# Kernel tuning notes

Measured on AMD Instinct MI355X. Metric: run time of the kernel, lower is better.

The kernel has to match this reference:

```python
import jax, jax.numpy as jnp
import numpy as np

N, E = 50000, 800000
IN_DIM, HID, HEADS, NUM_CLASSES, NUM_GRAPHS, NUM_LAYERS = 64, 64, 4, 10000, 256, 3
OUT_W = HID * HEADS  # 256


def _gat_layer(x, src, dst, W, a_src, a_dst, b, n_nodes):
    # x: [N, in], W: [heads*out, in], a_src/a_dst: [heads, out], b: [heads*out]
    h = (x @ W.T).reshape(n_nodes, HEADS, HID)            # [N, H, D]
    s_src = jnp.einsum('nhd,hd->nh', h, a_src)            # [N, H]
    s_dst = jnp.einsum('nhd,hd->nh', h, a_dst)
    alpha = jax.nn.leaky_relu(s_src[src] + s_dst[dst], 0.2)  # [E, H]
    m = jax.ops.segment_max(alpha, dst, num_segments=n_nodes)
    m = jnp.where(jnp.isfinite(m), m, 0.0)                # isolated-node safety
    ex = jnp.exp(alpha - m[dst])
    denom = jax.ops.segment_sum(ex, dst, num_segments=n_nodes)
    w = ex / (denom[dst] + 1e-16)                         # PyG softmax epsilon
    out = jax.ops.segment_sum(h[src] * w[:, :, None], dst, num_segments=n_nodes)
    return out.reshape(n_nodes, HEADS * HID) + b


def setup_inputs() -> dict:
    key = jax.random.key(0)
    ks = jax.random.split(key, 20)
    inp = {
        'x': jax.random.normal(ks[0], (N, IN_DIM), jnp.float32),
        'edge_index': jax.random.randint(ks[1], (2, E), 0, N, jnp.int32),
        'batch': jnp.sort(jax.random.randint(ks[2], (N,), 0, NUM_GRAPHS, jnp.int32)),
        'class_label': jax.random.randint(ks[3], (NUM_GRAPHS,), 0, NUM_CLASSES, jnp.int32),
        'emb': jax.random.normal(ks[4], (NUM_CLASSES, HID), jnp.float32),
    }
    in_dims = [IN_DIM + HID, OUT_W, OUT_W]
    for l in range(NUM_LAYERS):
        kw = jax.random.split(ks[5 + l], 4)
        d_in = in_dims[l]
        sc = 1.0 / np.sqrt(d_in)
        inp[f'W{l}'] = jax.random.uniform(kw[0], (OUT_W, d_in), jnp.float32, -sc, sc)
        inp[f'asrc{l}'] = jax.random.uniform(kw[1], (HEADS, HID), jnp.float32, -sc, sc)
        inp[f'adst{l}'] = jax.random.uniform(kw[2], (HEADS, HID), jnp.float32, -sc, sc)
        inp[f'b{l}'] = jnp.zeros((OUT_W,), jnp.float32)
    sc = 1.0 / np.sqrt(OUT_W)
    inp['cls_W'] = jax.random.uniform(ks[10], (1, OUT_W), jnp.float32, -sc, sc)
    inp['cls_b'] = jnp.zeros((1,), jnp.float32)
    return inp


def reference(x, edge_index, batch, class_label, emb,
              W0, asrc0, adst0, b0,
              W1, asrc1, adst1, b1,
              W2, asrc2, adst2, b2,
              cls_W, cls_b):
    n = x.shape[0]
    # template embedding aligned per node
    t = emb[class_label][batch]                          # [N, HID]
    h = jnp.concatenate([x, t], axis=-1)                 # [N, IN+HID]
    # PyG GATConv adds self-loops by default
    loop = jnp.arange(n, dtype=edge_index.dtype)
    src = jnp.concatenate([edge_index[0], loop])
    dst = jnp.concatenate([edge_index[1], loop])
    params = [(W0, asrc0, adst0, b0), (W1, asrc1, adst1, b1), (W2, asrc2, adst2, b2)]
    for (W, a_s, a_d, b) in params:
        h = _gat_layer(h, src, dst, W, a_s, a_d, b, n)
        h = jax.nn.leaky_relu(h, 0.01)                   # F.leaky_relu default slope
    return h @ cls_W.T + cls_b                           # [N, 1]
```

## Files before the change

kernel.cpp:

```cpp
#include <hip/hip_runtime.h>
#include <hip/hip_fp16.h>
#include <math.h>

#define NNODES 50000
#define NEDGES 800000
#define NT_TILES (((NNODES + 127) / 128) * 2)
#define NGROUPS ((NNODES + 3) / 4)
#define NH0 (NNODES * 128)
#define NH04 (NH0 / 4)
#define NW4 (163840 / 4)
#define NDEG4 (NNODES / 4)
#define NPREP4 (NH04 + NW4 + NDEG4)

typedef __attribute__((ext_vector_type(8))) _Float16 f16x8;
typedef __attribute__((ext_vector_type(4))) _Float16 f16x4;
typedef __attribute__((ext_vector_type(4))) float f32x4;

static __device__ __forceinline__ void gl_lds16(const void* g, void* l) {
    __builtin_amdgcn_global_load_lds(
        (const __attribute__((address_space(1))) void*)g,
        (__attribute__((address_space(3))) void*)l, 16, 0, 0);
}

static __device__ __forceinline__ float sel4(float4 v, int head) {
    float r = v.x;
    r = (head == 1) ? v.y : r;
    r = (head == 2) ? v.z : r;
    r = (head == 3) ? v.w : r;
    return r;
}

__global__ void prep_kernel(const float* __restrict__ x,
                            const int* __restrict__ batch,
                            const int* __restrict__ class_label,
                            const float* __restrict__ emb,
                            const float* __restrict__ W0,
                            const float* __restrict__ W1,
                            const float* __restrict__ W2,
                            _Float16* __restrict__ h0,
                            _Float16* __restrict__ F0,
                            _Float16* __restrict__ F1,
                            _Float16* __restrict__ F2,
                            int* __restrict__ deg) {
    int i4 = blockIdx.x * blockDim.x + threadIdx.x;
    if (i4 < NH04) {
        int idx = i4 * 4;
        int n = idx >> 7, c = idx & 127;
        float4 v;
        if (c < 64) v = *(const float4*)&x[(n << 6) + c];
        else        v = *(const float4*)&emb[class_label[batch[n]] * 64 + (c - 64)];
        f16x4 h = {(_Float16)v.x, (_Float16)v.y, (_Float16)v.z, (_Float16)v.w};
        *(f16x4*)&h0[idx] = h;
    } else if (i4 < NH04 + NW4) {
        int i = (i4 - NH04) * 4;
        const float* src; _Float16* dst;
        if (i < 32768)       { src = W0 + i;           dst = F0 + i; }
        else if (i < 98304)  { src = W1 + (i - 32768); dst = F1 + (i - 32768); }
        else                 { src = W2 + (i - 98304); dst = F2 + (i - 98304); }
        float4 v = *(const float4*)src;
        f16x4 h = {(_Float16)v.x, (_Float16)v.y, (_Float16)v.z, (_Float16)v.w};
        *(f16x4*)dst = h;
    } else if (i4 < NPREP4) {
        int j = (i4 - NH04 - NW4) * 4;
        int4 z = {0, 0, 0, 0};
        *(int4*)&deg[j] = z;
    }
}

template <int K>
static __device__ void gemm_tile_dev(const _Float16* __restrict__ A,
                                     const _Float16* __restrict__ W,
                                     const float* __restrict__ a_src,
                                     const float* __restrict__ a_dst,
                                     _Float16* __restrict__ Cf,
                                     float* __restrict__ ssrc,
                                     float* __restrict__ sdst,
                                     char* smem, int bm, int bn) {
    const int M = NNODES;
    int tid = threadIdx.x;
    int lane = tid & 63, wave = tid >> 6;
    int wm = wave >> 1, wn = wave & 1;
    int l16 = lane & 15, quad = lane >> 4;
    int rsub = lane >> 3;
    int kcs = (lane & 7) ^ rsub;
    int sw = l16 & 7;

    f32x4 acc[4][4];
#pragma unroll
    for (int r = 0; r < 4; ++r)
#pragma unroll
        for (int c = 0; c < 4; ++c) acc[r][c] = (f32x4){0.f, 0.f, 0.f, 0.f};

    const int NST = K / 64;
    auto issue = [&](int buf, int s) {
        _Float16* dA = (_Float16*)(smem + buf * 32768);
        _Float16* dB = (_Float16*)(smem + buf * 32768 + 16384);
        int ks = s * 64;
#pragma unroll
        for (int j = 0; j < 4; ++j) {
            int seg = wave * 4 + j;
            int r = seg * 8 + rsub;
            int acol = ks + kcs * 8;
            int garow = bm + r; if (garow > M - 1) garow = M - 1;
            gl_lds16(A + (size_t)garow * K + acol, &dA[seg * 512]);
            gl_lds16(W + (size_t)(bn + r) * K + acol, &dB[seg * 512]);
        }
    };

    issue(0, 0);
    __syncthreads();
#pragma unroll
    for (int s = 0; s < NST; ++s) {
        if (s + 1 < NST) issue((s + 1) & 1, s + 1);
        const _Float16* sA = (const _Float16*)(smem + (s & 1) * 32768);
        const _Float16* sB = (const _Float16*)(smem + (s & 1) * 32768 + 16384);
#pragma unroll
        for (int ks32 = 0; ks32 < 2; ++ks32) {
            f16x8 af[4], bf[4];
#pragma unroll
            for (int r = 0; r < 4; ++r) {
                int row = wm * 64 + r * 16 + l16;
                af[r] = *(const f16x8*)&sA[row * 64 + ((ks32 * 4 + quad) ^ sw) * 8];
            }
#pragma unroll
            for (int c = 0; c < 4; ++c) {
                int row = wn * 64 + c * 16 + l16;
                bf[c] = *(const f16x8*)&sB[row * 64 + ((ks32 * 4 + quad) ^ sw) * 8];
            }
#pragma unroll
            for (int r = 0; r < 4; ++r)
#pragma unroll
                for (int c = 0; c < 4; ++c)
                    acc[r][c] = __builtin_amdgcn_mfma_f32_16x16x32_f16(
                        bf[c], af[r], acc[r][c], 0, 0, 0);
        }
        __syncthreads();
    }

    int headblk = (bn + wn * 64) >> 6;
    f32x4 av[4], dv[4];
#pragma unroll
    for (int c = 0; c < 4; ++c) {
        av[c] = *(const f32x4*)&a_src[headblk * 64 + c * 16 + quad * 4];
        dv[c] = *(const f32x4*)&a_dst[headblk * 64 + c * 16 + quad * 4];
    }
#pragma unroll
    for (int r = 0; r < 4; ++r) {
        int grow = bm + wm * 64 + r * 16 + l16;
        bool ok = grow < M;
        float ps = 0.f, pd = 0.f;
#pragma unroll
        for (int c = 0; c < 4; ++c) {
            f32x4 a = acc[r][c];
            ps += a[0] * av[c][0] + a[1] * av[c][1]
                + a[2] * av[c][2] + a[3] * av[c][3];
            pd += a[0] * dv[c][0] + a[1] * dv[c][1]
                + a[2] * dv[c][2] + a[3] * dv[c][3];
            if (ok) {
                f16x4 hv = {(_Float16)a[0], (_Float16)a[1],
                            (_Float16)a[2], (_Float16)a[3]};
                *(f16x4*)&Cf[(size_t)grow * 256 + bn + wn * 64 + c * 16 + quad * 4] = hv;
            }
        }
        ps += __shfl_xor(ps, 16, 64);
        ps += __shfl_xor(ps, 32, 64);
        pd += __shfl_xor(pd, 16, 64);
        pd += __shfl_xor(pd, 32, 64);
        if (quad == 0 && ok) {
            ssrc[grow * 4 + headblk] = ps;
            sdst[grow * 4 + headblk] = pd;
        }
    }
}

template <int K>
__global__ __launch_bounds__(256) void gemm_mfma_kernel(
        const _Float16* __restrict__ A, const _Float16* __restrict__ W,
        const float* __restrict__ a_src, const float* __restrict__ a_dst,
        _Float16* __restrict__ Cf,
        float* __restrict__ ssrc, float* __restrict__ sdst) {
    __shared__ __align__(16) char smem[65536];
    gemm_tile_dev<K>(A, W, a_src, a_dst, Cf, ssrc, sdst, smem,
                     blockIdx.x * 128, blockIdx.y * 128);
}

__global__ __launch_bounds__(256) void gemm0_bucket_kernel(
        const _Float16* __restrict__ A, const _Float16* __restrict__ W,
        const float* __restrict__ a_src, const float* __restrict__ a_dst,
        _Float16* __restrict__ Cf,
        float* __restrict__ ssrc, float* __restrict__ sdst,
        const int* __restrict__ ei,
        int* __restrict__ deg, int* __restrict__ slots) {
    __shared__ __align__(16) char smem[65536];
    int b = blockIdx.x;
    if ((b & 1) == 0) {
        int tile = b >> 1;
        if (tile < NT_TILES)
            gemm_tile_dev<128>(A, W, a_src, a_dst, Cf, ssrc, sdst, smem,
                               (tile >> 1) * 128, (tile & 1) * 128);
    } else {
        int rel = b >> 1;
        int stride = NT_TILES * 256;
        for (int e = rel * 256 + (int)threadIdx.x; e < NEDGES; e += stride) {
            int d = ei[NEDGES + e];
            int pos = atomicAdd(&deg[d], 1);
            if (pos < 64) slots[(size_t)d * 64 + pos] = ei[e];
        }
    }
}

template <bool LAST>
__global__ __launch_bounds__(256) void aggregate_kernel(
        const _Float16* __restrict__ hpf,
        const float* __restrict__ ssrc,
        const float* __restrict__ sdst,
        const int* __restrict__ deg,
        const int* __restrict__ slots,
        const float* __restrict__ bias,
        _Float16* __restrict__ out_h,
        const float* __restrict__ cls_W,
        const float* __restrict__ cls_b,
        float* __restrict__ out) {
    __shared__ __align__(16) float s_w[4][64][4];
    __shared__ int s_idx[4][64];
    int lane = threadIdx.x & 63;
    int slot = threadIdx.x >> 6;
    int n = blockIdx.x * 4 + slot;
    if (n >= NNODES) return;
    int head = lane >> 4;
    int dn = deg[n]; if (dn > 64) dn = 64;
    float4 sd = ((const float4*)sdst)[n];
    const f16x4* hp4 = (const f16x4*)hpf;

    float4 ssl = ((const float4*)ssrc)[n];
    float ax = ssl.x + sd.x, ay = ssl.y + sd.y;
    float az = ssl.z + sd.z, aw = ssl.w + sd.w;
    ax = ax > 0.f ? ax : 0.2f * ax;
    ay = ay > 0.f ? ay : 0.2f * ay;
    az = az > 0.f ? az : 0.2f * az;
    aw = aw > 0.f ? aw : 0.2f * aw;
    float4 exs = {__expf(ax), __expf(ay), __expf(az), __expf(aw)};
    float wself = sel4(exs, head);
    f16x4 vs = hp4[(size_t)n * 64 + lane];
    float dsum = wself;
    float4 acc = {wself * (float)vs.x, wself * (float)vs.y,
                  wself * (float)vs.z, wself * (float)vs.w};

    float4 ex = {0.f, 0.f, 0.f, 0.f};
    int s = 0;
    if (lane < dn) {
        s = slots[(size_t)n * 64 + lane];
        float4 ss = ((const float4*)ssrc)[s];
        float bx = ss.x + sd.x, by = ss.y + sd.y;
        float bz = ss.z + sd.z, bw = ss.w + sd.w;
        bx = bx > 0.f ? bx : 0.2f * bx;
        by = by > 0.f ? by : 0.2f * by;
        bz = bz > 0.f ? bz : 0.2f * bz;
        bw = bw > 0.f ? bw : 0.2f * bw;
        ex.x = __expf(bx); ex.y = __expf(by);
        ex.z = __expf(bz); ex.w = __expf(bw);
    }
    *(float4*)&s_w[slot][lane][0] = ex;
    s_idx[slot][lane] = s;

    int e = 0;
    for (; e + 8 <= dn; e += 8) {
        int si[8]; float w[8]; f16x4 v[8];
#pragma unroll
        for (int t = 0; t < 8; ++t) {
            si[t] = s_idx[slot][e + t];
            w[t] = s_w[slot][e + t][head];
        }
#pragma unroll
        for (int t = 0; t < 8; ++t) v[t] = hp4[(size_t)si[t] * 64 + lane];
#pragma unroll
        for (int t = 0; t < 8; ++t) {
            dsum += w[t];
            acc.x += w[t] * (float)v[t].x;
            acc.y += w[t] * (float)v[t].y;
            acc.z += w[t] * (float)v[t].z;
            acc.w += w[t] * (float)v[t].w;
        }
    }
    for (; e < dn; ++e) {
        int si = s_idx[slot][e];
        float w = s_w[slot][e][head];
        f16x4 v = hp4[(size_t)si * 64 + lane];
        dsum += w;
        acc.x += w * (float)v.x; acc.y += w * (float)v.y;
        acc.z += w * (float)v.z; acc.w += w * (float)v.w;
    }

    float inv = 1.f / (dsum + 1e-16f);
    float4 bv = ((const float4*)bias)[lane];
    float4 o;
    o.x = acc.x * inv + bv.x;
    o.y = acc.y * inv + bv.y;
    o.z = acc.z * inv + bv.z;
    o.w = acc.w * inv + bv.w;
    o.x = o.x > 0.f ? o.x : 0.01f * o.x;
    o.y = o.y > 0.f ? o.y : 0.01f * o.y;
    o.z = o.z > 0.f ? o.z : 0.01f * o.z;
    o.w = o.w > 0.f ? o.w : 0.01f * o.w;

    if (!LAST) {
        f16x4 ov = {(_Float16)o.x, (_Float16)o.y, (_Float16)o.z, (_Float16)o.w};
        ((f16x4*)out_h)[(size_t)n * 64 + lane] = ov;
    } else {
        float4 wv = ((const float4*)cls_W)[lane];
        float sdot = o.x * wv.x + o.y * wv.y + o.z * wv.z + o.w * wv.w;
#pragma unroll
        for (int off = 1; off < 64; off <<= 1)
            sdot += __shfl_xor(sdot, off, 64);
        if (lane == 0) out[n] = sdot + cls_b[0];
    }
}

extern "C" void kernel_launch(void* const* d_in, const int* in_sizes, int n_in,
                              void* d_out, int out_size, void* d_ws, size_t ws_size,
                              hipStream_t stream) {
    const float* x     = (const float*)d_in[0];
    const int*   ei    = (const int*)d_in[1];
    const int*   batch = (const int*)d_in[2];
    const int*   clab  = (const int*)d_in[3];
    const float* emb   = (const float*)d_in[4];
    const float* W[3]    = {(const float*)d_in[5], (const float*)d_in[9],  (const float*)d_in[13]};
    const float* asrc[3] = {(const float*)d_in[6], (const float*)d_in[10], (const float*)d_in[14]};
    const float* adst[3] = {(const float*)d_in[7], (const float*)d_in[11], (const float*)d_in[15]};
    const float* bias[3] = {(const float*)d_in[8], (const float*)d_in[12], (const float*)d_in[16]};
    const float* clsW = (const float*)d_in[17];
    const float* clsb = (const float*)d_in[18];
    float* out = (float*)d_out;

    char* ws = (char*)d_ws;
    size_t off = 0;
    auto alloc = [&](size_t bytes) {
        void* p = ws + off;
        off += (bytes + 255) & ~(size_t)255;
        return p;
    };
    _Float16* Cf   = (_Float16*)alloc((size_t)NNODES * 256 * 2);
    _Float16* hA   = (_Float16*)alloc((size_t)NNODES * 256 * 2);
    _Float16* h0f  = (_Float16*)alloc((size_t)NNODES * 128 * 2);
    _Float16* Wf[3];
    Wf[0] = (_Float16*)alloc((size_t)256 * 128 * 2);
    Wf[1] = (_Float16*)alloc((size_t)256 * 256 * 2);
    Wf[2] = (_Float16*)alloc((size_t)256 * 256 * 2);
    float* ssrc  = (float*)alloc((size_t)NNODES * 4 * 4);
    float* sdst  = (float*)alloc((size_t)NNODES * 4 * 4);
    int*   deg   = (int*)alloc((size_t)NNODES * 4);
    int*   slots = (int*)alloc((size_t)NNODES * 64 * 4);
    (void)ws_size; (void)in_sizes; (void)n_in; (void)out_size;

    prep_kernel<<<dim3((NPREP4 + 255) / 256), dim3(256), 0, stream>>>(
        x, batch, clab, emb, W[0], W[1], W[2], h0f, Wf[0], Wf[1], Wf[2], deg);

    dim3 gemm_grid((NNODES + 127) / 128, 2);
    dim3 node_grid(NGROUPS);

    gemm0_bucket_kernel<<<dim3(NT_TILES * 2), dim3(256), 0, stream>>>(
        h0f, Wf[0], asrc[0], adst[0], Cf, ssrc, sdst, ei, deg, slots);
    aggregate_kernel<false><<<node_grid, dim3(256), 0, stream>>>(
        Cf, ssrc, sdst, deg, slots, bias[0], hA, nullptr, nullptr, nullptr);

    gemm_mfma_kernel<256><<<gemm_grid, dim3(256), 0, stream>>>(
        hA, Wf[1], asrc[1], adst[1], Cf, ssrc, sdst);
    aggregate_kernel<false><<<node_grid, dim3(256), 0, stream>>>(
        Cf, ssrc, sdst, deg, slots, bias[1], hA, nullptr, nullptr, nullptr);

    gemm_mfma_kernel<256><<<gemm_grid, dim3(256), 0, stream>>>(
        hA, Wf[2], asrc[2], adst[2], Cf, ssrc, sdst);
    aggregate_kernel<true><<<node_grid, dim3(256), 0, stream>>>(
        Cf, ssrc, sdst, deg, slots, bias[2], nullptr, clsW, clsb, out);
}
```

Baseline: 373.3 us.

## Software-pipeline neighbor gathers, precompute byte offsets in slots, raise occupancy hint

```diff
diff --git a/kernel.cpp b/kernel.cpp
--- a/kernel.cpp
+++ b/kernel.cpp
@@ -1,6 +1,7 @@
 #include <hip/hip_runtime.h>
 #include <hip/hip_fp16.h>
 #include <math.h>
+#include <stdint.h>
 
 #define NNODES 50000
 #define NEDGES 800000
@@ -204,13 +205,13 @@
         for (int e = rel * 256 + (int)threadIdx.x; e < NEDGES; e += stride) {
             int d = ei[NEDGES + e];
             int pos = atomicAdd(&deg[d], 1);
-            if (pos < 64) slots[(size_t)d * 64 + pos] = ei[e];
+            if (pos < 64) slots[(size_t)d * 64 + pos] = ei[e] << 9;
         }
     }
 }
 
 template <bool LAST>
-__global__ __launch_bounds__(256) void aggregate_kernel(
+__global__ __launch_bounds__(256, 8) void aggregate_kernel(
         const _Float16* __restrict__ hpf,
         const float* __restrict__ ssrc,
         const float* __restrict__ sdst,
@@ -228,9 +229,10 @@
     int n = blockIdx.x * 4 + slot;
     if (n >= NNODES) return;
     int head = lane >> 4;
+    uint32_t lane8 = (uint32_t)lane * 8u;
+    const char* hbase = (const char*)hpf;
     int dn = deg[n]; if (dn > 64) dn = 64;
     float4 sd = ((const float4*)sdst)[n];
-    const f16x4* hp4 = (const f16x4*)hpf;
 
     float4 ssl = ((const float4*)ssrc)[n];
     float ax = ssl.x + sd.x, ay = ssl.y + sd.y;
@@ -241,16 +243,16 @@
     aw = aw > 0.f ? aw : 0.2f * aw;
     float4 exs = {__expf(ax), __expf(ay), __expf(az), __expf(aw)};
     float wself = sel4(exs, head);
-    f16x4 vs = hp4[(size_t)n * 64 + lane];
+    f16x4 vs = *(const f16x4*)(hbase + (((uint32_t)n << 9) + lane8));
     float dsum = wself;
     float4 acc = {wself * (float)vs.x, wself * (float)vs.y,
                   wself * (float)vs.z, wself * (float)vs.w};
 
     float4 ex = {0.f, 0.f, 0.f, 0.f};
-    int s = 0;
+    int soff = 0;
     if (lane < dn) {
-        s = slots[(size_t)n * 64 + lane];
-        float4 ss = ((const float4*)ssrc)[s];
+        soff = slots[(size_t)n * 64 + lane];
+        float4 ss = *(const float4*)((const char*)ssrc + ((uint32_t)soff >> 5));
         float bx = ss.x + sd.x, by = ss.y + sd.y;
         float bz = ss.z + sd.z, bw = ss.w + sd.w;
         bx = bx > 0.f ? bx : 0.2f * bx;
@@ -261,34 +263,47 @@
         ex.z = __expf(bz); ex.w = __expf(bw);
     }
     *(float4*)&s_w[slot][lane][0] = ex;
-    s_idx[slot][lane] = s;
-
-    int e = 0;
-    for (; e + 8 <= dn; e += 8) {
-        int si[8]; float w[8]; f16x4 v[8];
+    s_idx[slot][lane] = soff;
+
+    auto loadb = [&](int eb, f16x4* v, float* w) {
 #pragma unroll
         for (int t = 0; t < 8; ++t) {
-            si[t] = s_idx[slot][e + t];
-            w[t] = s_w[slot][e + t][head];
-        }
-#pragma unroll
-        for (int t = 0; t < 8; ++t) v[t] = hp4[(size_t)si[t] * 64 + lane];
+            uint32_t off = (uint32_t)s_idx[slot][eb + t] + lane8;
+            v[t] = *(const f16x4*)(hbase + off);
+            w[t] = s_w[slot][eb + t][head];
+        }
+    };
+    auto accum = [&](const f16x4* v, const float* w) {
 #pragma unroll
         for (int t = 0; t < 8; ++t) {
-            dsum += w[t];
-            acc.x += w[t] * (float)v[t].x;
-            acc.y += w[t] * (float)v[t].y;
-            acc.z += w[t] * (float)v[t].z;
-            acc.w += w[t] * (float)v[t].w;
-        }
-    }
-    for (; e < dn; ++e) {
-        int si = s_idx[slot][e];
-        float w = s_w[slot][e][head];
-        f16x4 v = hp4[(size_t)si * 64 + lane];
-        dsum += w;
-        acc.x += w * (float)v.x; acc.y += w * (float)v.y;
-        acc.z += w * (float)v.z; acc.w += w * (float)v.w;
+            float wt = w[t];
+            dsum += wt;
+            acc.x += wt * (float)v[t].x;
+            acc.y += wt * (float)v[t].y;
+            acc.z += wt * (float)v[t].z;
+            acc.w += wt * (float)v[t].w;
+        }
+    };
+
+    int B = (dn + 7) >> 3;
+    if (B) {
+        f16x4 va[8], vb[8];
+        float wa[8], wb[8];
+        loadb(0, va, wa);
+        int i = 1;
+        for (; i + 1 < B; i += 2) {
+            loadb(i * 8, vb, wb);
+            accum(va, wa);
+            loadb((i + 1) * 8, va, wa);
+            accum(vb, wb);
+        }
+        if (i < B) {
+            loadb(i * 8, vb, wb);
+            accum(va, wa);
+            accum(vb, wb);
+        } else {
+            accum(va, wa);
+        }
     }
 
     float inv = 1.f / (dsum + 1e-16f);
```

Measured after the change: 408.5 us. 9.4% more time.

## Split aggregation into weight-packing and column-sliced gather kernels with sliced layout

Applied to the files above, without the earlier changes.

```diff
diff --git a/kernel.cpp b/kernel.cpp
--- a/kernel.cpp
+++ b/kernel.cpp
@@ -1,6 +1,7 @@
 #include <hip/hip_runtime.h>
 #include <hip/hip_fp16.h>
 #include <math.h>
+#include <stdint.h>
 
 #define NNODES 50000
 #define NEDGES 800000
@@ -10,7 +11,8 @@
 #define NH04 (NH0 / 4)
 #define NW4 (163840 / 4)
 #define NDEG4 (NNODES / 4)
-#define NPREP4 (NH04 + NW4 + NDEG4)
+#define NSELF4 (NNODES / 4)
+#define NPREP4 (NH04 + NW4 + NDEG4 + NSELF4)
 
 typedef __attribute__((ext_vector_type(8))) _Float16 f16x8;
 typedef __attribute__((ext_vector_type(4))) _Float16 f16x4;
@@ -20,14 +22,6 @@
     __builtin_amdgcn_global_load_lds(
         (const __attribute__((address_space(1))) void*)g,
         (__attribute__((address_space(3))) void*)l, 16, 0, 0);
-}
-
-static __device__ __forceinline__ float sel4(float4 v, int head) {
-    float r = v.x;
-    r = (head == 1) ? v.y : r;
-    r = (head == 2) ? v.z : r;
-    r = (head == 3) ? v.w : r;
-    return r;
 }
 
 __global__ void prep_kernel(const float* __restrict__ x,
@@ -41,7 +35,8 @@
                             _Float16* __restrict__ F0,
                             _Float16* __restrict__ F1,
                             _Float16* __restrict__ F2,
-                            int* __restrict__ deg) {
+                            int* __restrict__ deg,
+                            int* __restrict__ slots) {
     int i4 = blockIdx.x * blockDim.x + threadIdx.x;
     if (i4 < NH04) {
         int idx = i4 * 4;
@@ -60,10 +55,16 @@
         float4 v = *(const float4*)src;
         f16x4 h = {(_Float16)v.x, (_Float16)v.y, (_Float16)v.z, (_Float16)v.w};
         *(f16x4*)dst = h;
+    } else if (i4 < NH04 + NW4 + NDEG4) {
+        int j = (i4 - NH04 - NW4) * 4;
+        int4 o = {1, 1, 1, 1};
+        *(int4*)&deg[j] = o;
     } else if (i4 < NPREP4) {
-        int j = (i4 - NH04 - NW4) * 4;
-        int4 z = {0, 0, 0, 0};
-        *(int4*)&deg[j] = z;
+        int j = (i4 - NH04 - NW4 - NDEG4) * 4;
+        slots[(size_t)(j + 0) * 64] = j + 0;
+        slots[(size_t)(j + 1) * 64] = j + 1;
+        slots[(size_t)(j + 2) * 64] = j + 2;
+        slots[(size_t)(j + 3) * 64] = j + 3;
     }
 }
 
@@ -157,9 +158,10 @@
             pd += a[0] * dv[c][0] + a[1] * dv[c][1]
                 + a[2] * dv[c][2] + a[3] * dv[c][3];
             if (ok) {
+                int col = bn + wn * 64 + c * 16 + quad * 4;
                 f16x4 hv = {(_Float16)a[0], (_Float16)a[1],
                             (_Float16)a[2], (_Float16)a[3]};
-                *(f16x4*)&Cf[(size_t)grow * 256 + bn + wn * 64 + c * 16 + quad * 4] = hv;
+                *(f16x4*)&Cf[((size_t)(col >> 5) * NNODES + grow) * 32 + (col & 31)] = hv;
             }
         }
         ps += __shfl_xor(ps, 16, 64);
@@ -209,48 +211,26 @@
     }
 }
 
-template <bool LAST>
-__global__ __launch_bounds__(256) void aggregate_kernel(
-        const _Float16* __restrict__ hpf,
+__global__ __launch_bounds__(256) void weights_kernel(
         const float* __restrict__ ssrc,
         const float* __restrict__ sdst,
         const int* __restrict__ deg,
         const int* __restrict__ slots,
-        const float* __restrict__ bias,
-        _Float16* __restrict__ out_h,
-        const float* __restrict__ cls_W,
-        const float* __restrict__ cls_b,
-        float* __restrict__ out) {
-    __shared__ __align__(16) float s_w[4][64][4];
-    __shared__ int s_idx[4][64];
+        unsigned* __restrict__ pk,
+        float* __restrict__ out,
+        const float* __restrict__ cls_b) {
     int lane = threadIdx.x & 63;
-    int slot = threadIdx.x >> 6;
-    int n = blockIdx.x * 4 + slot;
-    if (n >= NNODES) return;
-    int head = lane >> 4;
+    int wv = threadIdx.x >> 6;
+    int n = blockIdx.x * 4 + wv;
     int dn = deg[n]; if (dn > 64) dn = 64;
+    int dnp = (dn + 7) & ~7;
     float4 sd = ((const float4*)sdst)[n];
-    const f16x4* hp4 = (const f16x4*)hpf;
-
-    float4 ssl = ((const float4*)ssrc)[n];
-    float ax = ssl.x + sd.x, ay = ssl.y + sd.y;
-    float az = ssl.z + sd.z, aw = ssl.w + sd.w;
-    ax = ax > 0.f ? ax : 0.2f * ax;
-    ay = ay > 0.f ? ay : 0.2f * ay;
-    az = az > 0.f ? az : 0.2f * az;
-    aw = aw > 0.f ? aw : 0.2f * aw;
-    float4 exs = {__expf(ax), __expf(ay), __expf(az), __expf(aw)};
-    float wself = sel4(exs, head);
-    f16x4 vs = hp4[(size_t)n * 64 + lane];
-    float dsum = wself;
-    float4 acc = {wself * (float)vs.x, wself * (float)vs.y,
-                  wself * (float)vs.z, wself * (float)vs.w};
 
     float4 ex = {0.f, 0.f, 0.f, 0.f};
-    int s = 0;
+    int id = 0;
     if (lane < dn) {
-        s = slots[(size_t)n * 64 + lane];
-        float4 ss = ((const float4*)ssrc)[s];
+        id = slots[(size_t)n * 64 + lane];
+        float4 ss = ((const float4*)ssrc)[id];
         float bx = ss.x + sd.x, by = ss.y + sd.y;
         float bz = ss.z + sd.z, bw = ss.w + sd.w;
         bx = bx > 0.f ? bx : 0.2f * bx;
@@ -260,59 +240,103 @@
         ex.x = __expf(bx); ex.y = __expf(by);
         ex.z = __expf(bz); ex.w = __expf(bw);
     }
-    *(float4*)&s_w[slot][lane][0] = ex;
-    s_idx[slot][lane] = s;
-
-    int e = 0;
-    for (; e + 8 <= dn; e += 8) {
-        int si[8]; float w[8]; f16x4 v[8];
-#pragma unroll
-        for (int t = 0; t < 8; ++t) {
-            si[t] = s_idx[slot][e + t];
-            w[t] = s_w[slot][e + t][head];
-        }
-#pragma unroll
-        for (int t = 0; t < 8; ++t) v[t] = hp4[(size_t)si[t] * 64 + lane];
-#pragma unroll
-        for (int t = 0; t < 8; ++t) {
-            dsum += w[t];
-            acc.x += w[t] * (float)v[t].x;
-            acc.y += w[t] * (float)v[t].y;
-            acc.z += w[t] * (float)v[t].z;
-            acc.w += w[t] * (float)v[t].w;
-        }
-    }
-    for (; e < dn; ++e) {
-        int si = s_idx[slot][e];
-        float w = s_w[slot][e][head];
-        f16x4 v = hp4[(size_t)si * 64 + lane];
-        dsum += w;
+    float4 t = ex;
+#pragma unroll
+    for (int off = 1; off < 64; off <<= 1) {
+        t.x += __shfl_xor(t.x, off, 64);
+        t.y += __shfl_xor(t.y, off, 64);
+        t.z += __shfl_xor(t.z, off, 64);
+        t.w += __shfl_xor(t.w, off, 64);
+    }
+    float4 inv = {65535.f / (t.x + 1e-16f), 65535.f / (t.y + 1e-16f),
+                  65535.f / (t.z + 1e-16f), 65535.f / (t.w + 1e-16f)};
+    if (lane < dnp) {
+        unsigned idh = ((unsigned)id) << 16;
+        size_t b4 = (size_t)n * 4 * 64 + lane;
+        pk[b4 + 0 * 64] = idh | (unsigned)(ex.x * inv.x + 0.5f);
+        pk[b4 + 1 * 64] = idh | (unsigned)(ex.y * inv.y + 0.5f);
+        pk[b4 + 2 * 64] = idh | (unsigned)(ex.z * inv.z + 0.5f);
+        pk[b4 + 3 * 64] = idh | (unsigned)(ex.w * inv.w + 0.5f);
+    }
+    if (out && lane == 0) out[n] = cls_b[0];
+}
+
+template <bool LAST>
+__global__ __launch_bounds__(256) void slice_agg_kernel(
+        const _Float16* __restrict__ pay,
+        const unsigned* __restrict__ pk,
+        const int* __restrict__ deg,
+        const float* __restrict__ bias,
+        _Float16* __restrict__ out_h,
+        const float* __restrict__ cls_W,
+        float* __restrict__ out) {
+    int lane = threadIdx.x & 63;
+    int wv = threadIdx.x >> 6;
+    int j = blockIdx.x & 7;
+    int n = ((blockIdx.x >> 3) << 2) + wv;
+    int h = j >> 1;
+    int fb = j << 5;
+    int es = lane >> 3, fl = lane & 7;
+    int dn = deg[n]; if (dn > 64) dn = 64;
+    int R = (dn + 7) >> 3;
+
+    unsigned pkv = 0;
+    if (lane < (R << 3)) pkv = pk[((size_t)n * 4 + h) * 64 + lane];
+    const char* base = (const char*)pay + (((size_t)j * NNODES) << 6);
+    unsigned flo = (unsigned)(fl << 3);
+
+    float4 acc = {0.f, 0.f, 0.f, 0.f};
+    f16x4 v0, v1; float w0 = 0.f, w1 = 0.f;
+    auto fetch = [&](int r, f16x4& v, float& w) {
+        unsigned pv = (unsigned)__shfl((int)pkv, (r << 3) + es, 64);
+        w = (float)(pv & 0xffffu);
+        v = *(const f16x4*)(base + ((pv >> 16) << 6) + flo);
+    };
+    auto accum = [&](const f16x4& v, float w) {
         acc.x += w * (float)v.x; acc.y += w * (float)v.y;
         acc.z += w * (float)v.z; acc.w += w * (float)v.w;
-    }
-
-    float inv = 1.f / (dsum + 1e-16f);
-    float4 bv = ((const float4*)bias)[lane];
+    };
+    fetch(0, v0, w0);
+    int r = 1;
+    for (; r + 1 < R; r += 2) {
+        fetch(r, v1, w1);     accum(v0, w0);
+        fetch(r + 1, v0, w0); accum(v1, w1);
+    }
+    if (r < R) { fetch(r, v1, w1); accum(v0, w0); accum(v1, w1); }
+    else       { accum(v0, w0); }
+
+#pragma unroll
+    for (int off = 8; off < 64; off <<= 1) {
+        acc.x += __shfl_xor(acc.x, off, 64);
+        acc.y += __shfl_xor(acc.y, off, 64);
+        acc.z += __shfl_xor(acc.z, off, 64);
+        acc.w += __shfl_xor(acc.w, off, 64);
+    }
+    const float sc = 1.f / 65535.f;
+    float4 bv = *(const float4*)&bias[fb + (fl << 2)];
     float4 o;
-    o.x = acc.x * inv + bv.x;
-    o.y = acc.y * inv + bv.y;
-    o.z = acc.z * inv + bv.z;
-    o.w = acc.w * inv + bv.w;
+    o.x = acc.x * sc + bv.x;
+    o.y = acc.y * sc + bv.y;
+    o.z = acc.z * sc + bv.z;
+    o.w = acc.w * sc + bv.w;
     o.x = o.x > 0.f ? o.x : 0.01f * o.x;
     o.y = o.y > 0.f ? o.y : 0.01f * o.y;
     o.z = o.z > 0.f ? o.z : 0.01f * o.z;
     o.w = o.w > 0.f ? o.w : 0.01f * o.w;
 
     if (!LAST) {
-        f16x4 ov = {(_Float16)o.x, (_Float16)o.y, (_Float16)o.z, (_Float16)o.w};
-        ((f16x4*)out_h)[(size_t)n * 64 + lane] = ov;
+        if (es == 0) {
+            f16x4 ov = {(_Float16)o.x, (_Float16)o.y,
+                        (_Float16)o.z, (_Float16)o.w};
+            *(f16x4*)&out_h[(size_t)n * 256 + fb + (fl << 2)] = ov;
+        }
     } else {
-        float4 wv = ((const float4*)cls_W)[lane];
-        float sdot = o.x * wv.x + o.y * wv.y + o.z * wv.z + o.w * wv.w;
-#pragma unroll
-        for (int off = 1; off < 64; off <<= 1)
-            sdot += __shfl_xor(sdot, off, 64);
-        if (lane == 0) out[n] = sdot + cls_b[0];
+        float4 wv4 = *(const float4*)&cls_W[fb + (fl << 2)];
+        float dot = o.x * wv4.x + o.y * wv4.y + o.z * wv4.z + o.w * wv4.w;
+        dot += __shfl_xor(dot, 1, 64);
+        dot += __shfl_xor(dot, 2, 64);
+        dot += __shfl_xor(dot, 4, 64);
+        if (lane == 0) atomicAdd(&out[n], dot);
     }
 }
 
@@ -350,26 +374,34 @@
     float* sdst  = (float*)alloc((size_t)NNODES * 4 * 4);
     int*   deg   = (int*)alloc((size_t)NNODES * 4);
     int*   slots = (int*)alloc((size_t)NNODES * 64 * 4);
+    unsigned* pk = (unsigned*)alloc((size_t)NNODES * 4 * 64 * 4);
     (void)ws_size; (void)in_sizes; (void)n_in; (void)out_size;
 
     prep_kernel<<<dim3((NPREP4 + 255) / 256), dim3(256), 0, stream>>>(
-        x, batch, clab, emb, W[0], W[1], W[2], h0f, Wf[0], Wf[1], Wf[2], deg);
+        x, batch, clab, emb, W[0], W[1], W[2], h0f, Wf[0], Wf[1], Wf[2], deg, slots);
 
     dim3 gemm_grid((NNODES + 127) / 128, 2);
-    dim3 node_grid(NGROUPS);
+    dim3 grpA(NGROUPS);
+    dim3 grpB(NGROUPS * 8);
 
     gemm0_bucket_kernel<<<dim3(NT_TILES * 2), dim3(256), 0, stream>>>(
         h0f, Wf[0], asrc[0], adst[0], Cf, ssrc, sdst, ei, deg, slots);
-    aggregate_kernel<false><<<node_grid, dim3(256), 0, stream>>>(
-        Cf, ssrc, sdst, deg, slots, bias[0], hA, nullptr, nullptr, nullptr);
+    weights_kernel<<<grpA, dim3(256), 0, stream>>>(
+        ssrc, sdst, deg, slots, pk, nullptr, nullptr);
+    slice_agg_kernel<false><<<grpB, dim3(256), 0, stream>>>(
+        Cf, pk, deg, bias[0], hA, nullptr, nullptr);
 
     gemm_mfma_kernel<256><<<gemm_grid, dim3(256), 0, stream>>>(
         hA, Wf[1], asrc[1], adst[1], Cf, ssrc, sdst);
-    aggregate_kernel<false><<<node_grid, dim3(256), 0, stream>>>(
-        Cf, ssrc, sdst, deg, slots, bias[1], hA, nullptr, nullptr, nullptr);
+    weights_kernel<<<grpA, dim3(256), 0, stream>>>(
+        ssrc, sdst, deg, slots, pk, nullptr, nullptr);
+    slice_agg_kernel<false><<<grpB, dim3(256), 0, stream>>>(
+        Cf, pk, deg, bias[1], hA, nullptr, nullptr);
 
     gemm_mfma_kernel<256><<<gemm_grid, dim3(256), 0, stream>>>(
         hA, Wf[2], asrc[2], adst[2], Cf, ssrc, sdst);
-    aggregate_kernel<true><<<node_grid, dim3(256), 0, stream>>>(
-        Cf, ssrc, sdst, deg, slots, bias[2], nullptr, clsW, clsb, out);
-}
+    weights_kernel<<<grpA, dim3(256), 0, stream>>>(
+        ssrc, sdst, deg, slots, pk, out, clsb);
+    slice_agg_kernel<true><<<grpB, dim3(256), 0, stream>>>(
+        Cf, pk, deg, bias[2], nullptr, clsW, out);
+}
```

After: 580.9 us. 55.6% more time.
